# Performance work log

Measured on AMD Instinct MI355X. Metric: run time of the kernel, lower is better.

Reference implementation:

```python
import jax, jax.numpy as jnp
import numpy as np

N, E, G = 30000, 240000, 1500
EMB, NODE_DIM, EDGE_DIM, TASKS = 300, 9, 3, 12
L_ENC, L_RAT = 5, 2
GAMMA, T_CON = 0.4, 0.2


def _w(key, shape, fan_in):
    return jax.random.normal(key, shape, jnp.float32) / np.float32(np.sqrt(fan_in))


def setup_inputs() -> dict:
    key = jax.random.key(0)
    ks = jax.random.split(key, 32)
    inp = {}
    inp['x'] = jax.random.normal(ks[0], (N, NODE_DIM), jnp.float32)
    inp['edge_attr'] = jax.random.normal(ks[1], (E, EDGE_DIM), jnp.float32)
    inp['edge_index'] = jax.random.randint(ks[2], (2, E), 0, N, jnp.int32)
    b = jnp.sort(jax.random.randint(ks[3], (N,), 0, G, jnp.int32))
    inp['batch'] = b.at[0].set(0).at[-1].set(G - 1)
    u = jax.random.uniform(ks[4], (N, 2), jnp.float32, 1e-6, 1.0 - 1e-6)
    inp['gumbel'] = -jnp.log(-jnp.log(u))  # standard Gumbel noise (tau=1)
    inp['perm'] = jax.random.permutation(ks[5], G).astype(jnp.int32)
    inp['W_enc'] = _w(ks[6], (NODE_DIM, EMB), NODE_DIM)
    inp['b_enc'] = jnp.zeros((EMB,), jnp.float32)
    inp['We_g'] = _w(ks[7], (L_ENC, EDGE_DIM, EMB), EDGE_DIM)
    inp['be_g'] = jnp.zeros((L_ENC, EMB), jnp.float32)
    inp['W1_g'] = _w(ks[8], (L_ENC, EMB, 2 * EMB), EMB)
    inp['b1_g'] = jnp.zeros((L_ENC, 2 * EMB), jnp.float32)
    inp['W2_g'] = _w(ks[9], (L_ENC, 2 * EMB, EMB), 2 * EMB)
    inp['b2_g'] = jnp.zeros((L_ENC, EMB), jnp.float32)
    inp['We_r'] = _w(ks[10], (L_RAT, EDGE_DIM, EMB), EDGE_DIM)
    inp['be_r'] = jnp.zeros((L_RAT, EMB), jnp.float32)
    inp['W1_r'] = _w(ks[11], (L_RAT, EMB, 2 * EMB), EMB)
    inp['b1_r'] = jnp.zeros((L_RAT, 2 * EMB), jnp.float32)
    inp['W2_r'] = _w(ks[12], (L_RAT, 2 * EMB, EMB), 2 * EMB)
    inp['b2_r'] = jnp.zeros((L_RAT, EMB), jnp.float32)
    inp['Wg1'] = _w(ks[13], (EMB, 2 * EMB), EMB)
    inp['bg1'] = jnp.zeros((2 * EMB,), jnp.float32)
    inp['Wg2'] = _w(ks[14], (2 * EMB, 2), 2 * EMB)
    inp['bg2'] = jnp.zeros((2,), jnp.float32)
    inp['Wp1'] = _w(ks[15], (EMB, 2 * EMB), EMB)
    inp['bp1'] = jnp.zeros((2 * EMB,), jnp.float32)
    inp['Wp2'] = _w(ks[16], (2 * EMB, TASKS), 2 * EMB)
    inp['bp2'] = jnp.zeros((TASKS,), jnp.float32)
    return inp


def _gin_stack(x, src, dst, edge_attr, We, be, W1, b1, W2, b2):
    # GIN-style message passing with edge features, residual, JK='last'.
    L = We.shape[0]
    for l in range(L):
        e = edge_attr @ We[l] + be[l]                               # [E, EMB]
        msg = jax.nn.relu(x[src] + e)                                # gather [E, EMB]
        agg = jax.ops.segment_sum(msg, dst, num_segments=x.shape[0])  # scatter [N, EMB]
        h = jax.nn.relu((agg + x) @ W1[l] + b1[l]) @ W2[l] + b2[l]
        if l < L - 1:
            h = jax.nn.relu(h)
        x = x + h  # residual
    return x


def _mlp2(h, Wa, ba, Wb, bb):
    # Linear -> (BN=identity in eval) -> ReLU -> (Dropout=identity) -> Linear
    return jax.nn.relu(h @ Wa + ba) @ Wb + bb


def _forward(x, edge_attr, gumbel, W_enc, b_enc, We_g, be_g, W1_g, b1_g, W2_g, b2_g,
             We_r, be_r, W1_r, b1_r, W2_r, b2_r, Wg1, bg1, Wg2, bg2, Wp1, bp1, Wp2, bp2,
             edge_index, batch, perm):
    src, dst = edge_index[0], edge_index[1]
    cnt = jnp.clip(jax.ops.segment_sum(jnp.ones((x.shape[0],), jnp.float32), batch, num_segments=G), 1.0)[:, None]

    def gmean(v):
        return jax.ops.segment_sum(v, batch, num_segments=G) / cnt

    x_feat = x @ W_enc + b_enc                                      # node encoder
    h_node = _gin_stack(x_feat, src, dst, edge_attr, We_g, be_g, W1_g, b1_g, W2_g, b2_g)
    x_rat = _gin_stack(x_feat, src, dst, edge_attr, We_r, be_r, W1_r, b1_r, W2_r, b2_r)

    gate_logits = _mlp2(x_rat, Wg1, bg1, Wg2, bg2)                  # [N, 2]
    gate = jax.nn.softmax(gate_logits + gumbel, axis=-1)[:, 1:2]     # gumbel-softmax (soft), keep last col

    h_r = gmean(gate * h_node)
    h_env = gmean((1.0 - gate) * h_node)
    r_num = jax.ops.segment_sum(gate, batch, num_segments=G) + 1e-8
    env_num = jax.ops.segment_sum(1.0 - gate, batch, num_segments=G) + 1e-8

    pred_rem = _mlp2(h_r, Wp1, bp1, Wp2, bp2)
    loss_reg = jnp.abs(r_num / (r_num + env_num) - GAMMA).mean()

    h_out = gmean(h_node)
    na = jnp.linalg.norm(h_r, axis=1)
    nb = jnp.linalg.norm(h_out, axis=1)
    nc = jnp.linalg.norm(h_env, axis=1)
    sim = jnp.exp((h_r @ h_out.T) / (na[:, None] * nb[None, :] + 1e-8) / T_CON)
    sim_cp = jnp.exp((h_r @ h_env.T) / (na[:, None] * nc[None, :] + 1e-8) / T_CON)
    pos = jnp.diagonal(sim)
    loss_con = -jnp.log(pos / (sim_cp.sum(axis=1) + pos)).mean()

    pred_rep = _mlp2(h_r + h_env[perm], Wp1, bp1, Wp2, bp2)
    return pred_rep, pred_rem, loss_reg, loss_con


def reference(x, edge_attr, gumbel, W_enc, b_enc, We_g, be_g, W1_g, b1_g, W2_g, b2_g,
              We_r, be_r, W1_r, b1_r, W2_r, b2_r, Wg1, bg1, Wg2, bg2, Wp1, bp1, Wp2, bp2,
              edge_index, batch, perm):
    return _forward(x, edge_attr, gumbel, W_enc, b_enc, We_g, be_g, W1_g, b1_g, W2_g, b2_g,
                    We_r, be_r, W1_r, b1_r, W2_r, b2_r, Wg1, bg1, Wg2, bg2, Wp1, bp1, Wp2, bp2,
                    edge_index, batch, perm)
```

## Files before the change

kernel.cpp:

```cpp
#include <hip/hip_runtime.h>
#include <hip/hip_bf16.h>

typedef __hip_bfloat16 bf16;
typedef __attribute__((ext_vector_type(8))) short bf16x8;
typedef __attribute__((ext_vector_type(4))) float f32x4;

#define NN 30000
#define NE 240000
#define NG 1500
#define EMB 300
#define HID 600
#define NTASK 12
#define CG 75
#define SEM 320
#define SHID 608

__device__ __forceinline__ float tof(bf16 v){ return __bfloat162float(v); }
__device__ __forceinline__ bf16  tob(float v){ return __float2bfloat16(v); }
__device__ __forceinline__ float b2f(unsigned short u){ return __uint_as_float(((unsigned)u)<<16); }

__global__ __launch_bounds__(256) void k_zero_i(int* __restrict__ p, int n){
    int i = blockIdx.x*256 + threadIdx.x;
    if (i < n) p[i] = 0;
}

__global__ __launch_bounds__(256) void k_hist(const int* __restrict__ dst, int* __restrict__ deg){
    int e = blockIdx.x*256 + threadIdx.x;
    if (e < NE) atomicAdd(&deg[dst[e]], 1);
}

__global__ __launch_bounds__(256) void k_scan256(const int* __restrict__ deg, int* __restrict__ indptr,
                                                 int* __restrict__ cursor){
    __shared__ int sums[256];
    int t = threadIdx.x;
    const int chunk = (NN + 255) / 256;
    int s0 = t*chunk, s1 = min(s0+chunk, NN);
    int s = 0;
    for (int i=s0;i<s1;i++) s += deg[i];
    sums[t] = s;
    __syncthreads();
    for (int off=1; off<256; off<<=1){
        int v = (t>=off) ? sums[t-off] : 0;
        __syncthreads();
        sums[t] += v;
        __syncthreads();
    }
    int base = (t>0) ? sums[t-1] : 0;
    for (int i=s0;i<s1;i++){ indptr[i]=base; cursor[i]=base; base += deg[i]; }
    if (t==0) indptr[NN] = NE;
}

__global__ __launch_bounds__(256) void k_scatter(const int* __restrict__ dst, int* __restrict__ cursor,
                                                 int* __restrict__ eid){
    int e = blockIdx.x*256 + threadIdx.x;
    if (e < NE){ int p = atomicAdd(&cursor[dst[e]], 1); eid[p] = e; }
}

__global__ __launch_bounds__(256) void k_eprep(const int* __restrict__ eid, const int* __restrict__ src,
                                               const float* __restrict__ eattr, float4* __restrict__ epack){
    int k = blockIdx.x*256 + threadIdx.x;
    if (k >= NE) return;
    int e = eid[k];
    float4 p;
    p.x = __int_as_float(src[e]);
    p.y = eattr[e*3]; p.z = eattr[e*3+1]; p.w = eattr[e*3+2];
    epack[k] = p;
}

__global__ __launch_bounds__(256) void k_gstart(const int* __restrict__ batch, int* __restrict__ gstart){
    int g = blockIdx.x*256 + threadIdx.x;
    if (g > NG) return;
    if (g == NG){ gstart[NG] = NN; return; }
    int lo=0, hi=NN;
    while (lo<hi){ int mid=(lo+hi)>>1; if (batch[mid] < g) lo=mid+1; else hi=mid; }
    gstart[g] = lo;
}

__global__ __launch_bounds__(256) void k_wprep(const float* __restrict__ W, bf16* __restrict__ Wt,
                                               int K, int Kp, int N){
    __shared__ float t[32][33];
    const float* Wz = W + (size_t)blockIdx.z*K*N;
    bf16* Wtz = Wt + (size_t)blockIdx.z*N*Kp;
    int n0 = blockIdx.x*32, k0 = blockIdx.y*32;
    int tx = threadIdx.x & 31, ty = threadIdx.x >> 5;
    #pragma unroll
    for (int i=0;i<4;i++){
        int k = k0 + ty + i*8, n = n0 + tx;
        t[ty+i*8][tx] = (k<K && n<N) ? Wz[(size_t)k*N+n] : 0.f;
    }
    __syncthreads();
    #pragma unroll
    for (int i=0;i<4;i++){
        int n = n0 + ty + i*8, k = k0 + tx;
        if (n<N && k<Kp) Wtz[(size_t)n*Kp+k] = tob(t[tx][ty+i*8]);
    }
}

__global__ __launch_bounds__(256) void k_encoder(const float* __restrict__ x, const float* __restrict__ W,
                                                 const float* __restrict__ b, bf16* __restrict__ cur){
    int idx = blockIdx.x*256 + threadIdx.x;
    if (idx >= NN*EMB) return;
    int n = idx / EMB, c = idx - n*EMB;
    float acc = b[c];
    #pragma unroll
    for (int k=0;k<9;k++) acc += x[n*9+k] * W[k*EMB+c];
    cur[(size_t)n*SEM + c] = tob(acc);
}

__global__ __launch_bounds__(256) void k_agg4(const bf16* __restrict__ cur, const float* __restrict__ We,
                      const float* __restrict__ be, const float4* __restrict__ epack,
                      const int* __restrict__ indptr, bf16* __restrict__ apx){
    int idx = blockIdx.x*256 + threadIdx.x;
    if (idx >= NN*CG) return;
    int n = idx / CG, cg = idx - n*CG;
    int c0 = cg*4;
    float w0[4], w1[4], w2[4], bbv[4], acc[4];
    #pragma unroll
    for (int j=0;j<4;j++){
        w0[j] = We[c0+j]; w1[j] = We[EMB+c0+j]; w2[j] = We[2*EMB+c0+j]; bbv[j] = be[c0+j];
    }
    ushort4 hs = *(const ushort4*)&cur[(size_t)n*SEM + c0];
    acc[0]=b2f(hs.x); acc[1]=b2f(hs.y); acc[2]=b2f(hs.z); acc[3]=b2f(hs.w);
    int k  = indptr[n], k1 = indptr[n+1];
    for (; k+2 <= k1; k += 2){
        float4 e0 = epack[k], e1 = epack[k+1];
        int s0 = __float_as_int(e0.x), s1 = __float_as_int(e1.x);
        ushort4 ha = *(const ushort4*)&cur[(size_t)s0*SEM + c0];
        ushort4 hb = *(const ushort4*)&cur[(size_t)s1*SEM + c0];
        float fa[4] = {b2f(ha.x), b2f(ha.y), b2f(ha.z), b2f(ha.w)};
        float fb[4] = {b2f(hb.x), b2f(hb.y), b2f(hb.z), b2f(hb.w)};
        #pragma unroll
        for (int j=0;j<4;j++){
            float va = fa[j] + e0.y*w0[j] + e0.z*w1[j] + e0.w*w2[j] + bbv[j];
            float vb = fb[j] + e1.y*w0[j] + e1.z*w1[j] + e1.w*w2[j] + bbv[j];
            acc[j] += fmaxf(va, 0.f) + fmaxf(vb, 0.f);
        }
    }
    if (k < k1){
        float4 e0 = epack[k];
        int s0 = __float_as_int(e0.x);
        ushort4 ha = *(const ushort4*)&cur[(size_t)s0*SEM + c0];
        float fa[4] = {b2f(ha.x), b2f(ha.y), b2f(ha.z), b2f(ha.w)};
        #pragma unroll
        for (int j=0;j<4;j++){
            float va = fa[j] + e0.y*w0[j] + e0.z*w1[j] + e0.w*w2[j] + bbv[j];
            acc[j] += fmaxf(va, 0.f);
        }
    }
    ushort4 o;
    o.x = __bfloat16_as_ushort(tob(acc[0]));
    o.y = __bfloat16_as_ushort(tob(acc[1]));
    o.z = __bfloat16_as_ushort(tob(acc[2]));
    o.w = __bfloat16_as_ushort(tob(acc[3]));
    *(ushort4*)&apx[(size_t)n*SEM + c0] = o;
}

__global__ __launch_bounds__(256) void k_gemm2(const bf16* __restrict__ A, const bf16* __restrict__ Bt,
        const float* __restrict__ bias, const bf16* __restrict__ R, bf16* __restrict__ C,
        int M, int N, int Kp, int ldc, int relu_out){
    __shared__ __align__(16) char ldsbuf[34816];
    short (*Asl)[64][8] = reinterpret_cast<short(*)[64][8]>(ldsbuf);
    short (*Bsl)[64][8] = reinterpret_cast<short(*)[64][8]>(ldsbuf + 8192);
    short* Ct = reinterpret_cast<short*>(ldsbuf);
    const int CS = 136;
    int tid = threadIdx.x;
    int wave = tid >> 6, lane = tid & 63;
    int wm = wave >> 1, wn = wave & 1;
    int m0 = blockIdx.y*128, n0 = blockIdx.x*128;

    int srow = tid >> 1;
    int sq   = (tid & 1) * 2;
    int grA = min(m0 + srow, M-1);
    int grB = min(n0 + srow, N-1);
    const bf16* pA = A  + (size_t)grA*Kp + sq*8;
    const bf16* pB = Bt + (size_t)grB*Kp + sq*8;
    short* ldsA0 = &Asl[srow>>4][ sq   *16 + (srow&15)][0];
    short* ldsA1 = &Asl[srow>>4][(sq+1)*16 + (srow&15)][0];
    short* ldsB0 = &Bsl[srow>>4][ sq   *16 + (srow&15)][0];
    short* ldsB1 = &Bsl[srow>>4][(sq+1)*16 + (srow&15)][0];

    f32x4 acc[4][4];
    #pragma unroll
    for (int i=0;i<4;i++){
        #pragma unroll
        for (int j=0;j<4;j++) acc[i][j] = (f32x4){0.f,0.f,0.f,0.f};
    }

    int KC = Kp >> 5;
    uint4 ra0 = *(const uint4*)(pA);
    uint4 ra1 = *(const uint4*)(pA + 8);
    uint4 rb0 = *(const uint4*)(pB);
    uint4 rb1 = *(const uint4*)(pB + 8);

    for (int kc=0; kc<KC; ++kc){
        *(uint4*)ldsA0 = ra0; *(uint4*)ldsA1 = ra1;
        *(uint4*)ldsB0 = rb0; *(uint4*)ldsB1 = rb1;
        __syncthreads();
        if (kc+1 < KC){
            const bf16* qA = pA + (kc+1)*32;
            const bf16* qB = pB + (kc+1)*32;
            ra0 = *(const uint4*)(qA); ra1 = *(const uint4*)(qA+8);
            rb0 = *(const uint4*)(qB); rb1 = *(const uint4*)(qB+8);
        }
        bf16x8 af[4], bfr[4];
        #pragma unroll
        for (int i=0;i<4;i++) af[i]  = *(const bf16x8*)&Asl[wm*4+i][lane][0];
        #pragma unroll
        for (int j=0;j<4;j++) bfr[j] = *(const bf16x8*)&Bsl[wn*4+j][lane][0];
        #pragma unroll
        for (int i=0;i<4;i++){
            #pragma unroll
            for (int j=0;j<4;j++)
                acc[i][j] = __builtin_amdgcn_mfma_f32_16x16x32_bf16(af[i], bfr[j], acc[i][j], 0, 0, 0);
        }
        __syncthreads();
    }

    int lq = lane >> 4, lr = lane & 15;
    #pragma unroll
    for (int i=0;i<4;i++){
        int rl = (wm*4+i)*16 + lq*4;
        #pragma unroll
        for (int j=0;j<4;j++){
            int cl = (wn*4+j)*16 + lr;
            float bv = bias[min(n0+cl, N-1)];
            #pragma unroll
            for (int r=0;r<4;r++){
                float v = acc[i][j][r] + bv;
                if (relu_out) v = fmaxf(v, 0.f);
                Ct[(rl+r)*CS + cl] = (short)__bfloat16_as_ushort(tob(v));
            }
        }
    }
    __syncthreads();
    #pragma unroll
    for (int p=0;p<8;p++){
        int rl = p*16 + (tid>>4);
        int cl = (tid&15)*8;
        int row = m0 + rl, col = n0 + cl;
        if (row < M && col < N){
            union { short s8[8]; uint4 v; } u;
            u.v = *(uint4*)&Ct[rl*CS + cl];
            if (R){
                const bf16* rp = &R[(size_t)row*ldc + col];
                #pragma unroll
                for (int e=0;e<8;e++){
                    float v = b2f((unsigned short)u.s8[e]) + tof(rp[e]);
                    u.s8[e] = (short)__bfloat16_as_ushort(tob(v));
                }
            }
            *(uint4*)&C[(size_t)row*ldc + col] = u.v;
        }
    }
}

__device__ __forceinline__ void stage_tile(const short* __restrict__ P, int RB, int K, int r0, int k0,
                                           short (*lds)[64][8], int tid){
    #pragma unroll
    for (int s=0;s<2;s++){
        int seg = tid*2+s;
        int row = seg>>2, q = seg&3;
        int gr = r0 + row;
        int gk = k0 + q*8;
        union { short s8[8]; uint4 v; } u;
        if (gr < RB && gk + 8 <= K){
            const uint2* p = (const uint2*)(P + (size_t)gr*K + gk);
            uint2 lo = p[0], hi = p[1];
            u.v.x = lo.x; u.v.y = lo.y; u.v.z = hi.x; u.v.w = hi.y;
        } else {
            #pragma unroll
            for (int j=0;j<8;j++){
                int kk = gk + j;
                u.s8[j] = (gr < RB && kk < K) ? P[(size_t)gr*K + kk] : (short)0;
            }
        }
        *(uint4*)&lds[row>>4][q*16 + (row&15)][0] = u.v;
    }
}

__global__ __launch_bounds__(256) void k_sim_mfma(const bf16* __restrict__ A, const bf16* __restrict__ Bt,
                      const float* __restrict__ na, const float* __restrict__ nc, float* __restrict__ C){
    __shared__ __align__(16) short Asl[8][64][8];
    __shared__ __align__(16) short Bsl[8][64][8];
    int tid = threadIdx.x;
    int wave = tid >> 6, lane = tid & 63;
    int wm = wave >> 1, wn = wave & 1;
    int m0 = blockIdx.y*128, n0 = blockIdx.x*128;
    f32x4 acc[4][4];
    #pragma unroll
    for (int i=0;i<4;i++){
        #pragma unroll
        for (int j=0;j<4;j++) acc[i][j] = (f32x4){0.f,0.f,0.f,0.f};
    }
    for (int k0=0; k0<SEM; k0+=32){
        stage_tile((const short*)A,  NG, SEM, m0, k0, Asl, tid);
        stage_tile((const short*)Bt, NG, SEM, n0, k0, Bsl, tid);
        __syncthreads();
        bf16x8 af[4], bfr[4];
        #pragma unroll
        for (int i=0;i<4;i++) af[i]  = *(const bf16x8*)&Asl[wm*4+i][lane][0];
        #pragma unroll
        for (int j=0;j<4;j++) bfr[j] = *(const bf16x8*)&Bsl[wn*4+j][lane][0];
        #pragma unroll
        for (int i=0;i<4;i++){
            #pragma unroll
            for (int j=0;j<4;j++)
                acc[i][j] = __builtin_amdgcn_mfma_f32_16x16x32_bf16(af[i], bfr[j], acc[i][j], 0, 0, 0);
        }
        __syncthreads();
    }
    int lq = lane >> 4, lr = lane & 15;
    #pragma unroll
    for (int i=0;i<4;i++){
        int rb = m0 + (wm*4+i)*16 + lq*4;
        #pragma unroll
        for (int j=0;j<4;j++){
            int col = n0 + (wn*4+j)*16 + lr;
            if (col >= NG) continue;
            float ncj = nc[col];
            #pragma unroll
            for (int r=0;r<4;r++){
                int row = rb + r;
                if (row >= NG) continue;
                C[(size_t)row*NG+col] = expf(acc[i][j][r] * 5.0f / (na[row]*ncj + 1e-8f));
            }
        }
    }
}

__global__ __launch_bounds__(256) void k_gate(const bf16* __restrict__ mid, const float* __restrict__ Wg2,
                      const float* __restrict__ bg2, const float* __restrict__ gumbel, float* __restrict__ gate){
    int gw = blockIdx.x*4 + (threadIdx.x >> 6);
    int lane = threadIdx.x & 63;
    if (gw >= NN) return;
    float s0=0.f, s1=0.f;
    for (int i=lane;i<HID;i+=64){
        float h = tof(mid[(size_t)gw*SHID+i]);
        s0 += h * Wg2[i*2];
        s1 += h * Wg2[i*2+1];
    }
    for (int off=32; off>0; off>>=1){ s0 += __shfl_down(s0, off); s1 += __shfl_down(s1, off); }
    if (lane==0){
        float l0 = s0 + bg2[0] + gumbel[gw*2];
        float l1 = s1 + bg2[1] + gumbel[gw*2+1];
        float m = fmaxf(l0,l1);
        float e0 = expf(l0-m), e1 = expf(l1-m);
        gate[gw] = e1/(e0+e1);
    }
}

__global__ __launch_bounds__(320) void k_pool(const bf16* __restrict__ h, const float* __restrict__ gate,
                      const int* __restrict__ gstart, float* __restrict__ sumh, float* __restrict__ sumgh){
    int g = blockIdx.x, c = threadIdx.x;
    if (c >= EMB) return;
    int n0 = gstart[g], n1 = gstart[g+1];
    float sh=0.f, sg=0.f;
    for (int n=n0;n<n1;n++){
        float v = tof(h[(size_t)n*SEM+c]);
        float gt = gate[n];
        sh += v; sg += gt*v;
    }
    sumh[g*EMB+c] = sh; sumgh[g*EMB+c] = sg;
}

__global__ __launch_bounds__(256) void k_rnum(const float* __restrict__ gate, const int* __restrict__ gstart,
                      float* __restrict__ rnum, float* __restrict__ cntf){
    int g = blockIdx.x*4 + (threadIdx.x >> 6);
    int lane = threadIdx.x & 63;
    if (g >= NG) return;
    int n0 = gstart[g], n1 = gstart[g+1];
    float s=0.f;
    for (int n=n0+lane;n<n1;n+=64) s += gate[n];
    for (int off=32; off>0; off>>=1) s += __shfl_down(s, off);
    if (lane==0){ rnum[g] = s; cntf[g] = (float)(n1-n0); }
}

__global__ __launch_bounds__(256) void k_mean(const float* __restrict__ sumh, const float* __restrict__ sumgh,
                      const float* __restrict__ cntf, float* __restrict__ hr, float* __restrict__ henv,
                      float* __restrict__ hout, bf16* __restrict__ hrb, bf16* __restrict__ henvb){
    int idx = blockIdx.x*256 + threadIdx.x;
    if (idx >= NG*SEM) return;
    int g = idx / SEM, c = idx - g*SEM;
    if (c < EMB){
        int o = g*EMB + c;
        float inv = 1.f / fmaxf(cntf[g], 1.f);
        float sh = sumh[o], sg = sumgh[o];
        float r = sg*inv, e = (sh-sg)*inv;
        hr[o] = r; henv[o] = e; hout[o] = sh*inv;
        hrb[idx] = tob(r); henvb[idx] = tob(e);
    } else {
        hrb[idx] = tob(0.f); henvb[idx] = tob(0.f);
    }
}

__global__ __launch_bounds__(256) void k_pbuild(const float* __restrict__ hr, const float* __restrict__ henv,
                      const int* __restrict__ perm, bf16* __restrict__ P){
    int idx = blockIdx.x*256 + threadIdx.x;
    if (idx >= NG*SEM) return;
    int g = idx / SEM, c = idx - g*SEM;
    if (c < EMB){
        float v = hr[g*EMB+c];
        P[idx] = tob(v);
        P[(size_t)(NG+g)*SEM + c] = tob(v + henv[(size_t)perm[g]*EMB + c]);
    } else {
        P[idx] = tob(0.f);
        P[(size_t)(NG+g)*SEM + c] = tob(0.f);
    }
}

__global__ __launch_bounds__(256) void k_norm(const float* __restrict__ hr, const float* __restrict__ henv,
                      const float* __restrict__ hout, float* __restrict__ na, float* __restrict__ nc,
                      float* __restrict__ pos){
    int g = blockIdx.x*4 + (threadIdx.x >> 6);
    int lane = threadIdx.x & 63;
    if (g >= NG) return;
    float srr=0.f, soo=0.f, see=0.f, sro=0.f;
    for (int c=lane;c<EMB;c+=64){
        float r=hr[g*EMB+c], o=hout[g*EMB+c], e=henv[g*EMB+c];
        srr += r*r; soo += o*o; see += e*e; sro += r*o;
    }
    for (int off=32; off>0; off>>=1){
        srr += __shfl_down(srr,off); soo += __shfl_down(soo,off);
        see += __shfl_down(see,off); sro += __shfl_down(sro,off);
    }
    if (lane==0){
        float a = sqrtf(srr), b = sqrtf(soo), c2 = sqrtf(see);
        na[g] = a; nc[g] = c2;
        pos[g] = expf(sro/(a*b + 1e-8f) * 5.0f);
    }
}

__global__ __launch_bounds__(256) void k_rowsum(const float* __restrict__ simcp, float* __restrict__ S){
    __shared__ float red[256];
    int g = blockIdx.x, t = threadIdx.x;
    float s = 0.f;
    for (int j=t;j<NG;j+=256) s += simcp[(size_t)g*NG+j];
    red[t]=s; __syncthreads();
    for (int off=128; off>0; off>>=1){ if (t<off) red[t]+=red[t+off]; __syncthreads(); }
    if (t==0) S[g]=red[0];
}

__global__ __launch_bounds__(256) void k_pred(const bf16* __restrict__ hidP, const float* __restrict__ Wp2,
                      const float* __restrict__ bp2, float* __restrict__ out){
    int r = blockIdx.x*4 + (threadIdx.x >> 6);
    int lane = threadIdx.x & 63;
    if (r >= 2*NG) return;
    float acc[NTASK];
    #pragma unroll
    for (int t=0;t<NTASK;t++) acc[t] = 0.f;
    for (int i=lane;i<HID;i+=64){
        float h = tof(hidP[(size_t)r*SHID+i]);
        const float4* wp = (const float4*)&Wp2[i*NTASK];
        float4 wa = wp[0], wb = wp[1], wc = wp[2];
        acc[0]+=h*wa.x; acc[1]+=h*wa.y; acc[2]+=h*wa.z; acc[3]+=h*wa.w;
        acc[4]+=h*wb.x; acc[5]+=h*wb.y; acc[6]+=h*wb.z; acc[7]+=h*wb.w;
        acc[8]+=h*wc.x; acc[9]+=h*wc.y; acc[10]+=h*wc.z; acc[11]+=h*wc.w;
    }
    #pragma unroll
    for (int t=0;t<NTASK;t++){
        for (int off=32; off>0; off>>=1) acc[t] += __shfl_down(acc[t], off);
    }
    if (lane==0){
        float* dst = (r < NG) ? &out[NG*NTASK + r*NTASK] : &out[(r-NG)*NTASK];
        #pragma unroll
        for (int t=0;t<NTASK;t++) dst[t] = acc[t] + bp2[t];
    }
}

__global__ __launch_bounds__(256) void k_loss(const float* __restrict__ cntf, const float* __restrict__ rnum,
                      const float* __restrict__ pos, const float* __restrict__ S, float* __restrict__ out){
    __shared__ float ra[256], rb[256];
    int t = threadIdx.x;
    float a=0.f, b=0.f;
    for (int g=t; g<NG; g+=256){
        float r = rnum[g] + 1e-8f;
        float e = (cntf[g] - rnum[g]) + 1e-8f;
        a += fabsf(r/(r+e) - 0.4f);
        float p = pos[g];
        b += -logf(p/(S[g]+p));
    }
    ra[t]=a; rb[t]=b; __syncthreads();
    for (int off=128; off>0; off>>=1){ if (t<off){ ra[t]+=ra[t+off]; rb[t]+=rb[t+off]; } __syncthreads(); }
    if (t==0){
        out[2*NG*NTASK]   = ra[0]/NG;
        out[2*NG*NTASK+1] = rb[0]/NG;
    }
}

extern "C" void kernel_launch(void* const* d_in, const int* in_sizes, int n_in,
                              void* d_out, int out_size, void* d_ws, size_t ws_size,
                              hipStream_t stream) {
    const float* x      = (const float*)d_in[0];
    const float* eattr  = (const float*)d_in[1];
    const int*   eidx   = (const int*)d_in[2];
    const int*   batch  = (const int*)d_in[3];
    const float* gumbel = (const float*)d_in[4];
    const int*   perm   = (const int*)d_in[5];
    const float* W_enc  = (const float*)d_in[6];
    const float* b_enc  = (const float*)d_in[7];
    const float* We_g   = (const float*)d_in[8];
    const float* be_g   = (const float*)d_in[9];
    const float* W1_g   = (const float*)d_in[10];
    const float* b1_g   = (const float*)d_in[11];
    const float* W2_g   = (const float*)d_in[12];
    const float* b2_g   = (const float*)d_in[13];
    const float* We_r   = (const float*)d_in[14];
    const float* be_r   = (const float*)d_in[15];
    const float* W1_r   = (const float*)d_in[16];
    const float* b1_r   = (const float*)d_in[17];
    const float* W2_r   = (const float*)d_in[18];
    const float* b2_r   = (const float*)d_in[19];
    const float* Wg1    = (const float*)d_in[20];
    const float* bg1    = (const float*)d_in[21];
    const float* Wg2    = (const float*)d_in[22];
    const float* bg2    = (const float*)d_in[23];
    const float* Wp1    = (const float*)d_in[24];
    const float* bp1    = (const float*)d_in[25];
    const float* Wp2    = (const float*)d_in[26];
    const float* bp2    = (const float*)d_in[27];
    float* out = (float*)d_out;

    const int* srcArr = eidx;
    const int* dstArr = eidx + NE;

    char* w = (char*)d_ws;
    size_t off = 0;
    auto alloc = [&](size_t bytes)->char*{ char* p = w + off; off += (bytes + 255) & ~(size_t)255; return p; };
    bf16* cur   = (bf16*)alloc((size_t)NN*SEM*2);
    bf16* apx   = (bf16*)alloc((size_t)NN*SEM*2);
    char* midc  = alloc((size_t)NN*SHID*2);
    bf16* mid   = (bf16*)midc;
    float* simcp = (float*)midc;
    bf16* Pbuf   = (bf16*)(midc + 12*1024*1024);
    bf16* hidP   = (bf16*)(midc + 20*1024*1024);
    bf16* wt1g  = (bf16*)alloc((size_t)5*HID*SEM*2);
    bf16* wt2g  = (bf16*)alloc((size_t)5*EMB*SHID*2);
    bf16* wt1r  = (bf16*)alloc((size_t)2*HID*SEM*2);
    bf16* wt2r  = (bf16*)alloc((size_t)2*EMB*SHID*2);
    bf16* wtg1  = (bf16*)alloc((size_t)HID*SEM*2);
    bf16* wtp1  = (bf16*)alloc((size_t)HID*SEM*2);
    float4* epack = (float4*)alloc((size_t)NE*16);
    float* gate  = (float*)alloc((size_t)NN*4);
    float* sumh  = (float*)alloc((size_t)NG*EMB*4);
    float* sumgh = (float*)alloc((size_t)NG*EMB*4);
    float* hr    = (float*)alloc((size_t)NG*EMB*4);
    float* henv  = (float*)alloc((size_t)NG*EMB*4);
    float* hout  = (float*)alloc((size_t)NG*EMB*4);
    bf16* hrb    = (bf16*)alloc((size_t)NG*SEM*2);
    bf16* henvb  = (bf16*)alloc((size_t)NG*SEM*2);
    float* rnum  = (float*)alloc(NG*4);
    float* cntf  = (float*)alloc(NG*4);
    float* na    = (float*)alloc(NG*4);
    float* ncv   = (float*)alloc(NG*4);
    float* pos   = (float*)alloc(NG*4);
    float* Ssum  = (float*)alloc(NG*4);
    int* deg     = (int*)alloc((size_t)NN*4);
    int* indptr  = (int*)alloc((size_t)(NN+1)*4);
    int* cursor  = (int*)alloc((size_t)NN*4);
    int* eid     = (int*)alloc((size_t)NE*4);
    int* gstart  = (int*)alloc((size_t)(NG+1)*4);

    const int NB_NE  = (NE+255)/256;
    const int NB_NC  = (NN*EMB+255)/256;
    const int NB_AG  = (NN*CG+255)/256;
    const int NB_GP  = (NG*SEM+255)/256;

    k_zero_i <<<(NN+255)/256, 256, 0, stream>>>(deg, NN);
    k_hist   <<<NB_NE, 256, 0, stream>>>(dstArr, deg);
    k_scan256<<<1, 256, 0, stream>>>(deg, indptr, cursor);
    k_scatter<<<NB_NE, 256, 0, stream>>>(dstArr, cursor, eid);
    k_eprep  <<<NB_NE, 256, 0, stream>>>(eid, srcArr, eattr, epack);
    k_gstart <<<(NG+256)/256, 256, 0, stream>>>(batch, gstart);

    {
        dim3 g1t((HID+31)/32, SEM/32, 5);
        dim3 g2t((EMB+31)/32, SHID/32, 5);
        k_wprep<<<g1t, 256, 0, stream>>>(W1_g, wt1g, EMB, SEM, HID);
        k_wprep<<<g2t, 256, 0, stream>>>(W2_g, wt2g, HID, SHID, EMB);
        dim3 g1t2((HID+31)/32, SEM/32, 2);
        dim3 g2t2((EMB+31)/32, SHID/32, 2);
        k_wprep<<<g1t2, 256, 0, stream>>>(W1_r, wt1r, EMB, SEM, HID);
        k_wprep<<<g2t2, 256, 0, stream>>>(W2_r, wt2r, HID, SHID, EMB);
        dim3 g1t1((HID+31)/32, SEM/32, 1);
        k_wprep<<<g1t1, 256, 0, stream>>>(Wg1, wtg1, EMB, SEM, HID);
        k_wprep<<<g1t1, 256, 0, stream>>>(Wp1, wtp1, EMB, SEM, HID);
    }

    dim3 gm1((HID+127)/128, (NN+127)/128);
    dim3 gm2((EMB+127)/128, (NN+127)/128);

    k_encoder<<<NB_NC, 256, 0, stream>>>(x, W_enc, b_enc, cur);
    for (int l=0; l<2; l++){
        k_agg4 <<<NB_AG, 256, 0, stream>>>(cur, We_r + l*3*EMB, be_r + l*EMB, epack, indptr, apx);
        k_gemm2<<<gm1, 256, 0, stream>>>(apx, wt1r + (size_t)l*HID*SEM, b1_r + l*HID, nullptr, mid,
                                         NN, HID, SEM, SHID, 1);
        k_gemm2<<<gm2, 256, 0, stream>>>(mid, wt2r + (size_t)l*EMB*SHID, b2_r + l*EMB, cur, cur,
                                         NN, EMB, SHID, SEM, (l<1)?1:0);
    }
    k_gemm2<<<gm1, 256, 0, stream>>>(cur, wtg1, bg1, nullptr, mid, NN, HID, SEM, SHID, 1);
    k_gate<<<NN/4, 256, 0, stream>>>(mid, Wg2, bg2, gumbel, gate);

    k_encoder<<<NB_NC, 256, 0, stream>>>(x, W_enc, b_enc, cur);
    for (int l=0; l<5; l++){
        k_agg4 <<<NB_AG, 256, 0, stream>>>(cur, We_g + l*3*EMB, be_g + l*EMB, epack, indptr, apx);
        k_gemm2<<<gm1, 256, 0, stream>>>(apx, wt1g + (size_t)l*HID*SEM, b1_g + l*HID, nullptr, mid,
                                         NN, HID, SEM, SHID, 1);
        k_gemm2<<<gm2, 256, 0, stream>>>(mid, wt2g + (size_t)l*EMB*SHID, b2_g + l*EMB, cur, cur,
                                         NN, EMB, SHID, SEM, (l<4)?1:0);
    }

    k_pool  <<<NG, 320, 0, stream>>>(cur, gate, gstart, sumh, sumgh);
    k_rnum  <<<(NG+3)/4, 256, 0, stream>>>(gate, gstart, rnum, cntf);
    k_mean  <<<NB_GP, 256, 0, stream>>>(sumh, sumgh, cntf, hr, henv, hout, hrb, henvb);
    k_pbuild<<<NB_GP, 256, 0, stream>>>(hr, henv, perm, Pbuf);
    k_norm  <<<(NG+3)/4, 256, 0, stream>>>(hr, henv, hout, na, ncv, pos);
    dim3 gsim((NG+127)/128, (NG+127)/128);
    k_sim_mfma<<<gsim, 256, 0, stream>>>(hrb, henvb, na, ncv, simcp);
    k_rowsum<<<NG, 256, 0, stream>>>(simcp, Ssum);
    dim3 gph((HID+127)/128, (2*NG+127)/128);
    k_gemm2<<<gph, 256, 0, stream>>>(Pbuf, wtp1, bp1, nullptr, hidP, 2*NG, HID, SEM, SHID, 1);
    k_pred  <<<(2*NG+3)/4, 256, 0, stream>>>(hidP, Wp2, bp2, out);
    k_loss  <<<1, 256, 0, stream>>>(cntf, rnum, pos, Ssum, out);
}
```

Baseline: 1.053 ms.

## Parallelize CSR scan, widen aggregation to 8 channels, reuse encoder output

The single-block serial scan becomes a three-phase multi-block scan (block reduce, scan of block sums, local scan plus offset). The edge aggregation kernel now handles 8 channels per thread with 16-byte loads, halving thread count and the per-thread edge-index loads. The node encoder runs once into a separate buffer that both GIN stacks read for their first layer, so the second encoder launch is dropped. The 8-channel tail reads padded columns 300..303, which relies on the padding being finite or zero.

```diff
diff --git a/kernel.cpp b/kernel.cpp
--- a/kernel.cpp
+++ b/kernel.cpp
@@ -11,9 +11,10 @@
 #define EMB 300
 #define HID 600
 #define NTASK 12
-#define CG 75
 #define SEM 320
 #define SHID 608
+#define CG8 38
+#define NBLK_SCAN 118
 
 __device__ __forceinline__ float tof(bf16 v){ return __bfloat162float(v); }
 __device__ __forceinline__ bf16  tob(float v){ return __float2bfloat16(v); }
@@ -29,25 +30,48 @@
     if (e < NE) atomicAdd(&deg[dst[e]], 1);
 }
 
-__global__ __launch_bounds__(256) void k_scan256(const int* __restrict__ deg, int* __restrict__ indptr,
-                                                 int* __restrict__ cursor){
-    __shared__ int sums[256];
+__global__ __launch_bounds__(256) void k_scanA(const int* __restrict__ deg, int* __restrict__ bsum){
+    __shared__ int red[256];
+    int b = blockIdx.x, t = threadIdx.x;
+    int i = b*256 + t;
+    red[t] = (i < NN) ? deg[i] : 0;
+    __syncthreads();
+    for (int off=128; off>0; off>>=1){ if (t<off) red[t]+=red[t+off]; __syncthreads(); }
+    if (t==0) bsum[b] = red[0];
+}
+
+__global__ __launch_bounds__(128) void k_scanB(const int* __restrict__ bsum, int* __restrict__ boff){
+    __shared__ int s[128];
     int t = threadIdx.x;
-    const int chunk = (NN + 255) / 256;
-    int s0 = t*chunk, s1 = min(s0+chunk, NN);
-    int s = 0;
-    for (int i=s0;i<s1;i++) s += deg[i];
-    sums[t] = s;
+    int v = (t < NBLK_SCAN) ? bsum[t] : 0;
+    s[t] = v;
+    __syncthreads();
+    for (int off=1; off<128; off<<=1){
+        int add = (t>=off) ? s[t-off] : 0;
+        __syncthreads();
+        s[t] += add;
+        __syncthreads();
+    }
+    if (t < NBLK_SCAN) boff[t] = s[t] - v;
+}
+
+__global__ __launch_bounds__(256) void k_scanC(const int* __restrict__ deg, const int* __restrict__ boff,
+                                               int* __restrict__ indptr, int* __restrict__ cursor){
+    __shared__ int s[256];
+    int b = blockIdx.x, t = threadIdx.x;
+    int i = b*256 + t;
+    int v = (i < NN) ? deg[i] : 0;
+    s[t] = v;
     __syncthreads();
     for (int off=1; off<256; off<<=1){
-        int v = (t>=off) ? sums[t-off] : 0;
-        __syncthreads();
-        sums[t] += v;
-        __syncthreads();
-    }
-    int base = (t>0) ? sums[t-1] : 0;
-    for (int i=s0;i<s1;i++){ indptr[i]=base; cursor[i]=base; base += deg[i]; }
-    if (t==0) indptr[NN] = NE;
+        int add = (t>=off) ? s[t-off] : 0;
+        __syncthreads();
+        s[t] += add;
+        __syncthreads();
+    }
+    int excl = s[t] - v + boff[b];
+    if (i < NN){ indptr[i] = excl; cursor[i] = excl; }
+    if (i == 0) indptr[NN] = NE;
 }
 
 __global__ __launch_bounds__(256) void k_scatter(const int* __restrict__ dst, int* __restrict__ cursor,
@@ -97,62 +121,66 @@
 }
 
 __global__ __launch_bounds__(256) void k_encoder(const float* __restrict__ x, const float* __restrict__ W,
-                                                 const float* __restrict__ b, bf16* __restrict__ cur){
+                                                 const float* __restrict__ b, bf16* __restrict__ xfeat){
     int idx = blockIdx.x*256 + threadIdx.x;
     if (idx >= NN*EMB) return;
     int n = idx / EMB, c = idx - n*EMB;
     float acc = b[c];
     #pragma unroll
     for (int k=0;k<9;k++) acc += x[n*9+k] * W[k*EMB+c];
-    cur[(size_t)n*SEM + c] = tob(acc);
-}
-
-__global__ __launch_bounds__(256) void k_agg4(const bf16* __restrict__ cur, const float* __restrict__ We,
+    xfeat[(size_t)n*SEM + c] = tob(acc);
+}
+
+__global__ __launch_bounds__(256) void k_agg8(const bf16* __restrict__ cur, const float* __restrict__ We,
                       const float* __restrict__ be, const float4* __restrict__ epack,
                       const int* __restrict__ indptr, bf16* __restrict__ apx){
     int idx = blockIdx.x*256 + threadIdx.x;
-    if (idx >= NN*CG) return;
-    int n = idx / CG, cg = idx - n*CG;
-    int c0 = cg*4;
-    float w0[4], w1[4], w2[4], bbv[4], acc[4];
-    #pragma unroll
-    for (int j=0;j<4;j++){
-        w0[j] = We[c0+j]; w1[j] = We[EMB+c0+j]; w2[j] = We[2*EMB+c0+j]; bbv[j] = be[c0+j];
-    }
-    ushort4 hs = *(const ushort4*)&cur[(size_t)n*SEM + c0];
-    acc[0]=b2f(hs.x); acc[1]=b2f(hs.y); acc[2]=b2f(hs.z); acc[3]=b2f(hs.w);
-    int k  = indptr[n], k1 = indptr[n+1];
+    if (idx >= NN*CG8) return;
+    int n = idx / CG8, cg = idx - n*CG8;
+    int c0 = cg*8;
+    float w0[8], w1[8], w2[8], bb[8], acc[8];
+    #pragma unroll
+    for (int j=0;j<8;j++){
+        int ch = c0 + j;
+        bool ok = ch < EMB;
+        w0[j] = ok ? We[ch]       : 0.f;
+        w1[j] = ok ? We[EMB+ch]   : 0.f;
+        w2[j] = ok ? We[2*EMB+ch] : 0.f;
+        bb[j] = ok ? be[ch]       : 0.f;
+    }
+    union { unsigned short s[8]; uint4 v; } us;
+    us.v = *(const uint4*)&cur[(size_t)n*SEM + c0];
+    #pragma unroll
+    for (int j=0;j<8;j++) acc[j] = b2f(us.s[j]);
+    int k = indptr[n], k1 = indptr[n+1];
     for (; k+2 <= k1; k += 2){
         float4 e0 = epack[k], e1 = epack[k+1];
         int s0 = __float_as_int(e0.x), s1 = __float_as_int(e1.x);
-        ushort4 ha = *(const ushort4*)&cur[(size_t)s0*SEM + c0];
-        ushort4 hb = *(const ushort4*)&cur[(size_t)s1*SEM + c0];
-        float fa[4] = {b2f(ha.x), b2f(ha.y), b2f(ha.z), b2f(ha.w)};
-        float fb[4] = {b2f(hb.x), b2f(hb.y), b2f(hb.z), b2f(hb.w)};
-        #pragma unroll
-        for (int j=0;j<4;j++){
-            float va = fa[j] + e0.y*w0[j] + e0.z*w1[j] + e0.w*w2[j] + bbv[j];
-            float vb = fb[j] + e1.y*w0[j] + e1.z*w1[j] + e1.w*w2[j] + bbv[j];
+        union { unsigned short s[8]; uint4 v; } ua, ub;
+        ua.v = *(const uint4*)&cur[(size_t)s0*SEM + c0];
+        ub.v = *(const uint4*)&cur[(size_t)s1*SEM + c0];
+        #pragma unroll
+        for (int j=0;j<8;j++){
+            float va = b2f(ua.s[j]) + e0.y*w0[j] + e0.z*w1[j] + e0.w*w2[j] + bb[j];
+            float vb = b2f(ub.s[j]) + e1.y*w0[j] + e1.z*w1[j] + e1.w*w2[j] + bb[j];
             acc[j] += fmaxf(va, 0.f) + fmaxf(vb, 0.f);
         }
     }
     if (k < k1){
         float4 e0 = epack[k];
         int s0 = __float_as_int(e0.x);
-        ushort4 ha = *(const ushort4*)&cur[(size_t)s0*SEM + c0];
-        float fa[4] = {b2f(ha.x), b2f(ha.y), b2f(ha.z), b2f(ha.w)};
-        #pragma unroll
-        for (int j=0;j<4;j++){
-            float va = fa[j] + e0.y*w0[j] + e0.z*w1[j] + e0.w*w2[j] + bbv[j];
+        union { unsigned short s[8]; uint4 v; } ua;
+        ua.v = *(const uint4*)&cur[(size_t)s0*SEM + c0];
+        #pragma unroll
+        for (int j=0;j<8;j++){
+            float va = b2f(ua.s[j]) + e0.y*w0[j] + e0.z*w1[j] + e0.w*w2[j] + bb[j];
             acc[j] += fmaxf(va, 0.f);
         }
     }
-    ushort4 o;
-    o.x = __bfloat16_as_ushort(tob(acc[0]));
-    o.y = __bfloat16_as_ushort(tob(acc[1]));
-    o.z = __bfloat16_as_ushort(tob(acc[2]));
-    o.w = __bfloat16_as_ushort(tob(acc[3]));
-    *(ushort4*)&apx[(size_t)n*SEM + c0] = o;
+    union { unsigned short s[8]; uint4 v; } uo;
+    #pragma unroll
+    for (int j=0;j<8;j++) uo.s[j] = __bfloat16_as_ushort(tob(acc[j]));
+    *(uint4*)&apx[(size_t)n*SEM + c0] = uo.v;
 }
 
 __global__ __launch_bounds__(256) void k_gemm2(const bf16* __restrict__ A, const bf16* __restrict__ Bt,
@@ -526,6 +554,7 @@
     char* w = (char*)d_ws;
     size_t off = 0;
     auto alloc = [&](size_t bytes)->char*{ char* p = w + off; off += (bytes + 255) & ~(size_t)255; return p; };
+    bf16* xfeat = (bf16*)alloc((size_t)NN*SEM*2);
     bf16* cur   = (bf16*)alloc((size_t)NN*SEM*2);
     bf16* apx   = (bf16*)alloc((size_t)NN*SEM*2);
     char* midc  = alloc((size_t)NN*SHID*2);
@@ -559,15 +588,19 @@
     int* cursor  = (int*)alloc((size_t)NN*4);
     int* eid     = (int*)alloc((size_t)NE*4);
     int* gstart  = (int*)alloc((size_t)(NG+1)*4);
+    int* bsum    = (int*)alloc((size_t)NBLK_SCAN*4);
+    int* boff    = (int*)alloc((size_t)NBLK_SCAN*4);
 
     const int NB_NE  = (NE+255)/256;
     const int NB_NC  = (NN*EMB+255)/256;
-    const int NB_AG  = (NN*CG+255)/256;
+    const int NB_AG  = (NN*CG8+255)/256;
     const int NB_GP  = (NG*SEM+255)/256;
 
     k_zero_i <<<(NN+255)/256, 256, 0, stream>>>(deg, NN);
     k_hist   <<<NB_NE, 256, 0, stream>>>(dstArr, deg);
-    k_scan256<<<1, 256, 0, stream>>>(deg, indptr, cursor);
+    k_scanA  <<<NBLK_SCAN, 256, 0, stream>>>(deg, bsum);
+    k_scanB  <<<1, 128, 0, stream>>>(bsum, boff);
+    k_scanC  <<<NBLK_SCAN, 256, 0, stream>>>(deg, boff, indptr, cursor);
     k_scatter<<<NB_NE, 256, 0, stream>>>(dstArr, cursor, eid);
     k_eprep  <<<NB_NE, 256, 0, stream>>>(eid, srcArr, eattr, epack);
     k_gstart <<<(NG+256)/256, 256, 0, stream>>>(batch, gstart);
@@ -589,23 +622,25 @@
     dim3 gm1((HID+127)/128, (NN+127)/128);
     dim3 gm2((EMB+127)/128, (NN+127)/128);
 
-    k_encoder<<<NB_NC, 256, 0, stream>>>(x, W_enc, b_enc, cur);
+    k_encoder<<<NB_NC, 256, 0, stream>>>(x, W_enc, b_enc, xfeat);
+
     for (int l=0; l<2; l++){
-        k_agg4 <<<NB_AG, 256, 0, stream>>>(cur, We_r + l*3*EMB, be_r + l*EMB, epack, indptr, apx);
+        const bf16* in = (l==0) ? xfeat : cur;
+        k_agg8 <<<NB_AG, 256, 0, stream>>>(in, We_r + l*3*EMB, be_r + l*EMB, epack, indptr, apx);
         k_gemm2<<<gm1, 256, 0, stream>>>(apx, wt1r + (size_t)l*HID*SEM, b1_r + l*HID, nullptr, mid,
                                          NN, HID, SEM, SHID, 1);
-        k_gemm2<<<gm2, 256, 0, stream>>>(mid, wt2r + (size_t)l*EMB*SHID, b2_r + l*EMB, cur, cur,
+        k_gemm2<<<gm2, 256, 0, stream>>>(mid, wt2r + (size_t)l*EMB*SHID, b2_r + l*EMB, in, cur,
                                          NN, EMB, SHID, SEM, (l<1)?1:0);
     }
     k_gemm2<<<gm1, 256, 0, stream>>>(cur, wtg1, bg1, nullptr, mid, NN, HID, SEM, SHID, 1);
     k_gate<<<NN/4, 256, 0, stream>>>(mid, Wg2, bg2, gumbel, gate);
 
-    k_encoder<<<NB_NC, 256, 0, stream>>>(x, W_enc, b_enc, cur);
     for (int l=0; l<5; l++){
-        k_agg4 <<<NB_AG, 256, 0, stream>>>(cur, We_g + l*3*EMB, be_g + l*EMB, epack, indptr, apx);
+        const bf16* in = (l==0) ? xfeat : cur;
+        k_agg8 <<<NB_AG, 256, 0, stream>>>(in, We_g + l*3*EMB, be_g + l*EMB, epack, indptr, apx);
         k_gemm2<<<gm1, 256, 0, stream>>>(apx, wt1g + (size_t)l*HID*SEM, b1_g + l*HID, nullptr, mid,
                                          NN, HID, SEM, SHID, 1);
-        k_gemm2<<<gm2, 256, 0, stream>>>(mid, wt2g + (size_t)l*EMB*SHID, b2_g + l*EMB, cur, cur,
+        k_gemm2<<<gm2, 256, 0, stream>>>(mid, wt2g + (size_t)l*EMB*SHID, b2_g + l*EMB, in, cur,
                                          NN, EMB, SHID, SEM, (l<4)?1:0);
     }
 
```

Measured after the change: 1.305 ms. 1.24x slower.
